# Optimization experiments

Hardware: AMD Instinct MI355X
Metric: run time of the kernel (lower is better)

The kernel has to match this reference:

```python
import jax, jax.numpy as jnp
import numpy as np

NUM_CLASSES = 2
LOG2_NC = float(np.log2(NUM_CLASSES))


def _conv(x, w, b=None):
    # NCHW conv, stride 1, SAME padding (kernel 3 pad 1 or kernel 1 pad 0)
    y = jax.lax.conv_general_dilated(x, w, (1, 1), 'SAME',
                                     dimension_numbers=('NCHW', 'OIHW', 'NCHW'))
    if b is not None:
        y = y + b[None, :, None, None]
    return y


def _uncertainty_map(ds):
    # entropy over class dim, thresholded to {0,1}
    logp = jax.nn.log_softmax(ds, axis=1)            # [B,C,H,W]
    prob = jnp.exp(logp)
    # torch uses log2(prob + 1e-6); replicate exactly
    ent = -jnp.sum(prob * jnp.log2(prob + 1e-6), axis=1) / LOG2_NC  # [B,H,W]
    return (ent >= 0.001).astype(jnp.float32)


def _unob(tar, amap):
    # vectorized UnoB with S=3: interior pixels with tar!=0 get pro=0 unless
    # 4*tar == sum of the 4-neighborhood (i.e. locally constant label)
    t = tar  # [B,H,W] int
    nb = t[:, 2:, 1:-1] + t[:, :-2, 1:-1] + t[:, 1:-1, 2:] + t[:, 1:-1, :-2]
    center = t[:, 1:-1, 1:-1]
    inner_pro = jnp.where((center != 0) & (4 * center != nb), 0.0, 1.0)
    pro = jnp.ones_like(amap)
    pro = pro.at[:, 1:-1, 1:-1].set(inner_pro)
    return amap * pro


def setup_inputs() -> dict:
    key = jax.random.key(0)
    ks = jax.random.split(key, 6)
    B, C, H, W = 8, 128, 128, 128
    return {
        'x': jax.random.normal(ks[0], (B, C, H, W), jnp.float32),
        'skip': jax.random.normal(ks[1], (B, C, H, W), jnp.float32),
        'tar': jax.random.randint(ks[2], (B, 1, H, W), 0, NUM_CLASSES, jnp.int64)
            if jax.config.jax_enable_x64 else
            jax.random.randint(ks[2], (B, 1, H, W), 0, NUM_CLASSES).astype(jnp.int32),
        'W1': jax.random.normal(ks[3], (128, 256, 3, 3), jnp.float32) * 0.05,
        'b1': jnp.zeros((128,), jnp.float32),
        'W2': jax.random.normal(ks[4], (128, 128, 3, 3), jnp.float32) * 0.05,
        'b2': jnp.zeros((128,), jnp.float32),
        'Wds': jax.random.normal(ks[5], (NUM_CLASSES, 128, 1, 1), jnp.float32) * 0.05,
    }


def reference(x, skip, tar, W1, b1, W2, b2, Wds):
    h = jnp.concatenate([x, skip], axis=1)            # [B,2*dim,H,W]
    h = jax.nn.leaky_relu(_conv(h, W1, b1), 0.01)     # [B,dim,H,W]
    h = jax.nn.leaky_relu(_conv(h, W2, b2), 0.01)
    ds = _conv(h, Wds)                                # [B,num_classes,H,W]
    amap = _uncertainty_map(ds)                       # [B,H,W]
    amap = _unob(tar[:, 0], amap)                     # UnoB refinement, S=3
    return h, ds, amap
```

## Files before the change

### kernel.cpp

```cpp
#include <hip/hip_runtime.h>

typedef float f32x16 __attribute__((ext_vector_type(16)));
typedef short bf16x8 __attribute__((ext_vector_type(8)));
typedef unsigned int u32;

static __device__ __forceinline__ unsigned short f2bf(float f) {
  union { float f; unsigned int u; } v;
  v.f = f;
  return (unsigned short)((v.u + 0x7FFFu + ((v.u >> 16) & 1u)) >> 16);
}

static __device__ __forceinline__ void gl_lds16(const unsigned short* g,
                                                unsigned short* l) {
  __builtin_amdgcn_global_load_lds(
      (const __attribute__((address_space(1))) u32*)g,
      (__attribute__((address_space(3))) u32*)l, 16, 0, 0);
}

#define VMCNT8 asm volatile("s_waitcnt vmcnt(8)" ::: "memory")
#define VMCNT0 asm volatile("s_waitcnt vmcnt(0)" ::: "memory")
#define LGKM0 asm volatile("s_waitcnt lgkmcnt(0)" ::: "memory")
#define BAR __builtin_amdgcn_s_barrier()
#define SCHEDB __builtin_amdgcn_sched_barrier(0)
#define PRIO1 __builtin_amdgcn_s_setprio(1)
#define PRIO0 __builtin_amdgcn_s_setprio(0)

__global__ __launch_bounds__(256) void convert_weights(
    const float* __restrict__ W1, const float* __restrict__ W2,
    unsigned short* __restrict__ W1b, unsigned short* __restrict__ W2b,
    unsigned short* __restrict__ zp) {
  if (blockIdx.x == 1728) {
    uint4* z = (uint4*)zp;
    z[threadIdx.x] = make_uint4(0, 0, 0, 0);
    z[256 + threadIdx.x] = make_uint4(0, 0, 0, 0);
    return;
  }
  int i = blockIdx.x * 256 + threadIdx.x;
  if (i < 294912) {
    int e = i & 7, co = (i >> 3) & 127, r = i >> 10;
    int tap = r % 9, pc = r / 9;
    int ci = (pc >> 1) * 16 + (pc & 1) * 8 + e;
    W1b[i] = f2bf(W1[(co * 256 + ci) * 9 + tap]);
  } else {
    int j = i - 294912;
    if (j < 147456) {
      int e = j & 7, co = (j >> 3) & 127, r = j >> 10;
      int tap = r % 9, pc = r / 9;
      int ci = (pc >> 1) * 16 + (pc & 1) * 8 + e;
      W2b[j] = f2bf(W2[(co * 128 + ci) * 9 + tap]);
    }
  }
}

__global__ __launch_bounds__(256) void transpose_to_bf16(
    const float* __restrict__ src, unsigned short* __restrict__ dst, int cigb) {
  int row = blockIdx.x;
  int b = row >> 7, y = row & 127;
  const float* s = src + (long)b * 128 * 16384 + (long)y * 128;
  for (int it = 0; it < 8; ++it) {
    int u = it * 256 + (int)threadIdx.x;
    int cig = u >> 7, px = u & 127;
    unsigned short pk[8];
#pragma unroll
    for (int e = 0; e < 8; ++e)
      pk[e] = f2bf(s[(long)(cig * 8 + e) * 16384 + px]);
    uint4 vv;
    vv.x = (unsigned)pk[0] | ((unsigned)pk[1] << 16);
    vv.y = (unsigned)pk[2] | ((unsigned)pk[3] << 16);
    vv.z = (unsigned)pk[4] | ((unsigned)pk[5] << 16);
    vv.w = (unsigned)pk[6] | ((unsigned)pk[7] << 16);
    *(uint4*)(&dst[(((long)row * 32 + cigb + cig) * 130 + px + 1) * 8]) = vv;
  }
  if (cigb == 0 && threadIdx.x < 64) {
    int g = threadIdx.x >> 1;
    long col = (threadIdx.x & 1) * 129L;
    *(uint4*)(&dst[(((long)row * 32 + g) * 130 + col) * 8]) = make_uint4(0, 0, 0, 0);
  }
}

template <int CIN, bool FUSE_DS>
__global__ __launch_bounds__(512, 2) void conv3x3(
    const unsigned short* __restrict__ src,
    const unsigned short* __restrict__ wt,
    const float* __restrict__ bias,
    const unsigned short* __restrict__ zp,
    unsigned short* __restrict__ dst_bf16,
    float* __restrict__ dst_f32,
    const float* __restrict__ wds,
    const int* __restrict__ tar,
    float* __restrict__ ds,
    float* __restrict__ amap) {
  constexpr int CPG = CIN / 8;
  constexpr int NC = CIN / 16;
  __shared__ unsigned short in_tile[2][1664 * 8];
  __shared__ unsigned short wt_tile[2][2304 * 8];
  __shared__ unsigned short scr[64 * 8];
  __shared__ float sb[128];
  __shared__ float w0s[128], w1s[128];
  __shared__ float sc[4 * 4 * 2 * 32];

  const int tid = threadIdx.x;
  const int b = blockIdx.x >> 5;
  const int y0 = (blockIdx.x & 31) * 4;
  const int lane = tid & 63, wave = tid >> 6;
  const int wco = wave & 1, wrow = wave >> 1;
  const int l31 = lane & 31, kh = lane >> 5;

  if (tid < 128) {
    sb[tid] = bias[tid];
    if constexpr (FUSE_DS) {
      w0s[tid] = wds[tid];
      w1s[tid] = wds[128 + tid];
    }
  }

  const unsigned short* gb[8];
  unsigned short* ld0[8];
  int gst[8];
  int lst[8];
#pragma unroll
  for (int i = 0; i < 8; ++i) {
    const int o = wave * 8 + i;
    if (o < 36) {
      gb[i] = wt + o * 512 + lane * 8;
      gst[i] = 18432;
      ld0[i] = &wt_tile[0][(size_t)o * 512];
      lst[i] = 18432;
    } else if (o < 62) {
      const int q = o - 36;
      const int p = q / 13, j = q - p * 13;
      const int s = j * 64 + lane;
      const int hy = s / 130, hx = s - hy * 130;
      const int gy = y0 - 1 + hy;
      const bool ok = (s < 780) && (gy >= 0) && (gy < 128);
      gb[i] = ok ? src + ((size_t)((b * 128 + gy) * CPG) + p) * 1040 + hx * 8
                 : zp + lane * 8;
      gst[i] = ok ? 2080 : 0;
      ld0[i] = &in_tile[0][(size_t)(p * 832 + j * 64) * 8];
      lst[i] = 1664 * 8;
    } else {
      gb[i] = zp + lane * 8;
      gst[i] = 0;
      ld0[i] = &scr[0];
      lst[i] = 0;
    }
  }

  f32x16 acc[2][4] = {};

#pragma unroll
  for (int i = 0; i < 8; ++i) gl_lds16(gb[i], ld0[i]);
  VMCNT0;
  LGKM0;
  BAR;
  SCHEDB;

  for (int cic = 0; cic < NC; ++cic) {
    const int cur = cic & 1;
    const bool more = (cic + 1 < NC);
    if (more) {
      const int nb = cur ^ 1;
#pragma unroll
      for (int i = 0; i < 8; ++i)
        gl_lds16(gb[i] + (size_t)(cic + 1) * gst[i],
                 ld0[i] + (size_t)nb * lst[i]);
      SCHEDB;
      VMCNT8;
    } else {
      VMCNT0;
    }
    SCHEDB;
    BAR;
    SCHEDB;

    const unsigned short* it = &in_tile[cur][0];
    const unsigned short* wl = &wt_tile[cur][0];
    const size_t ib = (size_t)kh * (832 * 8);
    const size_t wb = (size_t)kh * 9216;

    bf16x8 xa0, xa1, xb0, xb1, xb2, xb3;
    bf16x8 ya0, ya1, yb0, yb1, yb2, yb3;

#define LD_TAP(T, A0, A1, B0, B1, B2, B3)                                      \
  {                                                                            \
    constexpr int ky_ = (T) / 3, kx_ = (T) % 3;                                \
    const int hy_ = ky_ + wrow;                                                \
    A0 = *(const bf16x8*)(&wl[wb + (size_t)((T)*128 + wco * 64 + l31) * 8]);   \
    A1 = *(const bf16x8*)(&wl[wb + (size_t)((T)*128 + wco * 64 + 32 + l31) * 8]); \
    B0 = *(const bf16x8*)(&it[ib + (size_t)(hy_ * 130 + l31 + kx_) * 8]);      \
    B1 = *(const bf16x8*)(&it[ib + (size_t)(hy_ * 130 + 32 + l31 + kx_) * 8]); \
    B2 = *(const bf16x8*)(&it[ib + (size_t)(hy_ * 130 + 64 + l31 + kx_) * 8]); \
    B3 = *(const bf16x8*)(&it[ib + (size_t)(hy_ * 130 + 96 + l31 + kx_) * 8]); \
  }

#define MFMA_TAP(A0, A1, B0, B1, B2, B3)                                       \
  {                                                                            \
    PRIO1;                                                                     \
    acc[0][0] = __builtin_amdgcn_mfma_f32_32x32x16_bf16(A0, B0, acc[0][0], 0, 0, 0); \
    acc[0][1] = __builtin_amdgcn_mfma_f32_32x32x16_bf16(A0, B1, acc[0][1], 0, 0, 0); \
    acc[0][2] = __builtin_amdgcn_mfma_f32_32x32x16_bf16(A0, B2, acc[0][2], 0, 0, 0); \
    acc[0][3] = __builtin_amdgcn_mfma_f32_32x32x16_bf16(A0, B3, acc[0][3], 0, 0, 0); \
    acc[1][0] = __builtin_amdgcn_mfma_f32_32x32x16_bf16(A1, B0, acc[1][0], 0, 0, 0); \
    acc[1][1] = __builtin_amdgcn_mfma_f32_32x32x16_bf16(A1, B1, acc[1][1], 0, 0, 0); \
    acc[1][2] = __builtin_amdgcn_mfma_f32_32x32x16_bf16(A1, B2, acc[1][2], 0, 0, 0); \
    acc[1][3] = __builtin_amdgcn_mfma_f32_32x32x16_bf16(A1, B3, acc[1][3], 0, 0, 0); \
    PRIO0;                                                                     \
  }

    LD_TAP(0, xa0, xa1, xb0, xb1, xb2, xb3);
    LD_TAP(1, ya0, ya1, yb0, yb1, yb2, yb3);
    SCHEDB;
    MFMA_TAP(xa0, xa1, xb0, xb1, xb2, xb3);
    LD_TAP(2, xa0, xa1, xb0, xb1, xb2, xb3);
    SCHEDB;
    MFMA_TAP(ya0, ya1, yb0, yb1, yb2, yb3);
    LD_TAP(3, ya0, ya1, yb0, yb1, yb2, yb3);
    SCHEDB;
    MFMA_TAP(xa0, xa1, xb0, xb1, xb2, xb3);
    LD_TAP(4, xa0, xa1, xb0, xb1, xb2, xb3);
    SCHEDB;
    MFMA_TAP(ya0, ya1, yb0, yb1, yb2, yb3);
    LD_TAP(5, ya0, ya1, yb0, yb1, yb2, yb3);
    SCHEDB;
    MFMA_TAP(xa0, xa1, xb0, xb1, xb2, xb3);
    LD_TAP(6, xa0, xa1, xb0, xb1, xb2, xb3);
    SCHEDB;
    MFMA_TAP(ya0, ya1, yb0, yb1, yb2, yb3);
    LD_TAP(7, ya0, ya1, yb0, yb1, yb2, yb3);
    SCHEDB;
    MFMA_TAP(xa0, xa1, xb0, xb1, xb2, xb3);
    LD_TAP(8, xa0, xa1, xb0, xb1, xb2, xb3);
    SCHEDB;
    MFMA_TAP(ya0, ya1, yb0, yb1, yb2, yb3);
    SCHEDB;
    MFMA_TAP(xa0, xa1, xb0, xb1, xb2, xb3);
#undef LD_TAP
#undef MFMA_TAP

    SCHEDB;
    LGKM0;
    BAR;
    SCHEDB;
  }

  const int gyo = y0 + wrow;
  float pd[4][2] = {};
#pragma unroll
  for (int fc = 0; fc < 2; ++fc) {
#pragma unroll
    for (int fp = 0; fp < 4; ++fp) {
      const int px = fp * 32 + l31;
      if constexpr (!FUSE_DS) {
#pragma unroll
        for (int rg = 0; rg < 4; ++rg) {
          const int co0 = wco * 64 + fc * 32 + rg * 8 + kh * 4;
          unsigned short pk[4];
#pragma unroll
          for (int q = 0; q < 4; ++q) {
            float v = acc[fc][fp][rg * 4 + q] + sb[co0 + q];
            v = v > 0.f ? v : 0.01f * v;
            pk[q] = f2bf(v);
          }
          uint2 o;
          o.x = (unsigned)pk[0] | ((unsigned)pk[1] << 16);
          o.y = (unsigned)pk[2] | ((unsigned)pk[3] << 16);
          *(uint2*)(&dst_bf16[(((long)(b * 128 + gyo) * 16 + (co0 >> 3)) * 130 + px + 1) * 8 +
                              kh * 4]) = o;
        }
      } else {
#pragma unroll
        for (int rg = 0; rg < 4; ++rg) {
          const int co0 = wco * 64 + fc * 32 + rg * 8 + kh * 4;
          float4 wv0 = *(const float4*)(&w0s[co0]);
          float4 wv1 = *(const float4*)(&w1s[co0]);
#pragma unroll
          for (int q = 0; q < 4; ++q) {
            float v = acc[fc][fp][rg * 4 + q] + sb[co0 + q];
            v = v > 0.f ? v : 0.01f * v;
            dst_f32[((long)(b * 128 + co0 + q) << 14) + (gyo << 7) + px] = v;
            float wq0 = (q == 0) ? wv0.x : (q == 1) ? wv0.y : (q == 2) ? wv0.z : wv0.w;
            float wq1 = (q == 0) ? wv1.x : (q == 1) ? wv1.y : (q == 2) ? wv1.z : wv1.w;
            pd[fp][0] += wq0 * v;
            pd[fp][1] += wq1 * v;
          }
        }
      }
    }
  }

  if constexpr (!FUSE_DS) {
    if (tid < 128) {
      int row = tid >> 5, g = (tid >> 1) & 15;
      long col = (tid & 1) * 129L;
      *(uint4*)(&dst_bf16[(((long)(b * 128 + y0 + row) * 16 + g) * 130 + col) * 8]) =
          make_uint4(0, 0, 0, 0);
    }
  } else {
#pragma unroll
    for (int fp = 0; fp < 4; ++fp)
#pragma unroll
      for (int c = 0; c < 2; ++c)
        pd[fp][c] += __shfl_xor(pd[fp][c], 32, 64);
    if (wco == 1 && kh == 0) {
#pragma unroll
      for (int fp = 0; fp < 4; ++fp)
#pragma unroll
        for (int c = 0; c < 2; ++c)
          sc[((wrow * 4 + fp) * 2 + c) * 32 + l31] = pd[fp][c];
    }
    __syncthreads();
    if (wco == 0 && kh == 0) {
      const int* tb = tar + (long)b * 16384;
#pragma unroll
      for (int fp = 0; fp < 4; ++fp) {
        const int px = fp * 32 + l31;
        float a0 = pd[fp][0] + sc[((wrow * 4 + fp) * 2 + 0) * 32 + l31];
        float a1 = pd[fp][1] + sc[((wrow * 4 + fp) * 2 + 1) * 32 + l31];
        ds[((long)b * 2) * 16384 + (gyo << 7) + px] = a0;
        ds[((long)b * 2 + 1) * 16384 + (gyo << 7) + px] = a1;
        float m = fmaxf(a0, a1);
        float e0 = expf(a0 - m), e1 = expf(a1 - m);
        float s = e0 + e1;
        float p0f = e0 / s, p1f = e1 / s;
        float ent = -(p0f * log2f(p0f + 1e-6f) + p1f * log2f(p1f + 1e-6f));
        float un = ent >= 0.001f ? 1.f : 0.f;
        float pro = 1.f;
        if (gyo > 0 && gyo < 127 && px > 0 && px < 127) {
          int c = tb[(gyo << 7) + px];
          if (c != 0) {
            int nb2 = tb[((gyo - 1) << 7) + px] + tb[((gyo + 1) << 7) + px] +
                      tb[(gyo << 7) + px - 1] + tb[(gyo << 7) + px + 1];
            if (4 * c != nb2) pro = 0.f;
          }
        }
        amap[((long)(b * 128 + gyo) << 7) + px] = un * pro;
      }
    }
  }
}

extern "C" void kernel_launch(void* const* d_in, const int* in_sizes, int n_in,
                              void* d_out, int out_size, void* d_ws, size_t ws_size,
                              hipStream_t stream) {
  const float* x    = (const float*)d_in[0];
  const float* skip = (const float*)d_in[1];
  const int*   tar  = (const int*)d_in[2];
  const float* W1   = (const float*)d_in[3];
  const float* b1   = (const float*)d_in[4];
  const float* W2   = (const float*)d_in[5];
  const float* b2   = (const float*)d_in[6];
  const float* Wds  = (const float*)d_in[7];

  float* out_h  = (float*)d_out;
  float* out_ds = out_h + 16777216;
  float* out_am = out_ds + 262144;

  unsigned short* W1b = (unsigned short*)d_ws;
  unsigned short* W2b = W1b + 294912;
  unsigned short* zp  = W2b + 147456;
  unsigned short* h1  = (unsigned short*)((char*)d_ws + (1u << 20));

  unsigned short* h0 = (unsigned short*)d_out;

  convert_weights<<<1729, 256, 0, stream>>>(W1, W2, W1b, W2b, zp);
  transpose_to_bf16<<<1024, 256, 0, stream>>>(x, h0, 0);
  transpose_to_bf16<<<1024, 256, 0, stream>>>(skip, h0, 16);
  conv3x3<256, false><<<256, 512, 0, stream>>>(h0, W1b, b1, zp, h1, nullptr,
                                               nullptr, nullptr, nullptr, nullptr);
  conv3x3<128, true><<<256, 512, 0, stream>>>(h1, W2b, b2, zp, nullptr, out_h,
                                              Wds, tar, out_ds, out_am);
}
```

Before: 149.3 us.

## Restructure conv prefetch pipeline, merge transpose launches, remap workgroups across XCDs

The next chunk's global-to-LDS prefetch now goes out in two halves interleaved with the MFMA taps. Barriers sit between tap groups and the wait for outstanding loads moves to the end of the iteration, so load latency hides behind compute. The two transpose launches are merged into one grid, and conv workgroup IDs are permuted so that adjacent rows of the same batch land on the same XCD. The extra barriers and the changed priority placement add synchronisation cost per iteration.

```diff
diff --git a/kernel.cpp b/kernel.cpp
--- a/kernel.cpp
+++ b/kernel.cpp
@@ -17,7 +17,6 @@
       (__attribute__((address_space(3))) u32*)l, 16, 0, 0);
 }
 
-#define VMCNT8 asm volatile("s_waitcnt vmcnt(8)" ::: "memory")
 #define VMCNT0 asm volatile("s_waitcnt vmcnt(0)" ::: "memory")
 #define LGKM0 asm volatile("s_waitcnt lgkmcnt(0)" ::: "memory")
 #define BAR __builtin_amdgcn_s_barrier()
@@ -53,8 +52,12 @@
 }
 
 __global__ __launch_bounds__(256) void transpose_to_bf16(
-    const float* __restrict__ src, unsigned short* __restrict__ dst, int cigb) {
-  int row = blockIdx.x;
+    const float* __restrict__ x, const float* __restrict__ skip,
+    unsigned short* __restrict__ dst) {
+  int bid = blockIdx.x;
+  const float* src = (bid < 1024) ? x : skip;
+  int cigb = (bid < 1024) ? 0 : 16;
+  int row = bid & 1023;
   int b = row >> 7, y = row & 127;
   const float* s = src + (long)b * 128 * 16384 + (long)y * 128;
   for (int it = 0; it < 8; ++it) {
@@ -100,8 +103,9 @@
   __shared__ float sc[4 * 4 * 2 * 32];
 
   const int tid = threadIdx.x;
-  const int b = blockIdx.x >> 5;
-  const int y0 = (blockIdx.x & 31) * 4;
+  const int wg = (blockIdx.x & 7) * 32 + (blockIdx.x >> 3);
+  const int b = wg >> 5;
+  const int y0 = (wg & 31) * 4;
   const int lane = tid & 63, wave = tid >> 6;
   const int wco = wave & 1, wrow = wave >> 1;
   const int l31 = lane & 31, kh = lane >> 5;
@@ -157,21 +161,8 @@
 
   for (int cic = 0; cic < NC; ++cic) {
     const int cur = cic & 1;
+    const int nbuf = cur ^ 1;
     const bool more = (cic + 1 < NC);
-    if (more) {
-      const int nb = cur ^ 1;
-#pragma unroll
-      for (int i = 0; i < 8; ++i)
-        gl_lds16(gb[i] + (size_t)(cic + 1) * gst[i],
-                 ld0[i] + (size_t)nb * lst[i]);
-      SCHEDB;
-      VMCNT8;
-    } else {
-      VMCNT0;
-    }
-    SCHEDB;
-    BAR;
-    SCHEDB;
 
     const unsigned short* it = &in_tile[cur][0];
     const unsigned short* wl = &wt_tile[cur][0];
@@ -195,7 +186,6 @@
 
 #define MFMA_TAP(A0, A1, B0, B1, B2, B3)                                       \
   {                                                                            \
-    PRIO1;                                                                     \
     acc[0][0] = __builtin_amdgcn_mfma_f32_32x32x16_bf16(A0, B0, acc[0][0], 0, 0, 0); \
     acc[0][1] = __builtin_amdgcn_mfma_f32_32x32x16_bf16(A0, B1, acc[0][1], 0, 0, 0); \
     acc[0][2] = __builtin_amdgcn_mfma_f32_32x32x16_bf16(A0, B2, acc[0][2], 0, 0, 0); \
@@ -204,12 +194,21 @@
     acc[1][1] = __builtin_amdgcn_mfma_f32_32x32x16_bf16(A1, B1, acc[1][1], 0, 0, 0); \
     acc[1][2] = __builtin_amdgcn_mfma_f32_32x32x16_bf16(A1, B2, acc[1][2], 0, 0, 0); \
     acc[1][3] = __builtin_amdgcn_mfma_f32_32x32x16_bf16(A1, B3, acc[1][3], 0, 0, 0); \
-    PRIO0;                                                                     \
   }
 
     LD_TAP(0, xa0, xa1, xb0, xb1, xb2, xb3);
     LD_TAP(1, ya0, ya1, yb0, yb1, yb2, yb3);
     SCHEDB;
+
+    if (more) {
+#pragma unroll
+      for (int i = 0; i < 4; ++i)
+        gl_lds16(gb[i] + (size_t)(cic + 1) * gst[i],
+                 ld0[i] + (size_t)nbuf * lst[i]);
+    }
+    SCHEDB;
+    BAR;
+    PRIO1;
     MFMA_TAP(xa0, xa1, xb0, xb1, xb2, xb3);
     LD_TAP(2, xa0, xa1, xb0, xb1, xb2, xb3);
     SCHEDB;
@@ -219,6 +218,17 @@
     MFMA_TAP(xa0, xa1, xb0, xb1, xb2, xb3);
     LD_TAP(4, xa0, xa1, xb0, xb1, xb2, xb3);
     SCHEDB;
+    PRIO0;
+
+    if (more) {
+#pragma unroll
+      for (int i = 4; i < 8; ++i)
+        gl_lds16(gb[i] + (size_t)(cic + 1) * gst[i],
+                 ld0[i] + (size_t)nbuf * lst[i]);
+    }
+    SCHEDB;
+    BAR;
+    PRIO1;
     MFMA_TAP(ya0, ya1, yb0, yb1, yb2, yb3);
     LD_TAP(5, ya0, ya1, yb0, yb1, yb2, yb3);
     SCHEDB;
@@ -228,17 +238,23 @@
     MFMA_TAP(ya0, ya1, yb0, yb1, yb2, yb3);
     LD_TAP(7, ya0, ya1, yb0, yb1, yb2, yb3);
     SCHEDB;
+    PRIO0;
+
+    BAR;
+    PRIO1;
     MFMA_TAP(xa0, xa1, xb0, xb1, xb2, xb3);
     LD_TAP(8, xa0, xa1, xb0, xb1, xb2, xb3);
     SCHEDB;
     MFMA_TAP(ya0, ya1, yb0, yb1, yb2, yb3);
     SCHEDB;
     MFMA_TAP(xa0, xa1, xb0, xb1, xb2, xb3);
+    PRIO0;
 #undef LD_TAP
 #undef MFMA_TAP
 
     SCHEDB;
     LGKM0;
+    VMCNT0;
     BAR;
     SCHEDB;
   }
@@ -363,8 +379,7 @@
   unsigned short* h0 = (unsigned short*)d_out;
 
   convert_weights<<<1729, 256, 0, stream>>>(W1, W2, W1b, W2b, zp);
-  transpose_to_bf16<<<1024, 256, 0, stream>>>(x, h0, 0);
-  transpose_to_bf16<<<1024, 256, 0, stream>>>(skip, h0, 16);
+  transpose_to_bf16<<<2048, 256, 0, stream>>>(x, skip, h0);
   conv3x3<256, false><<<256, 512, 0, stream>>>(h0, W1b, b1, zp, h1, nullptr,
                                                nullptr, nullptr, nullptr, nullptr);
   conv3x3<128, true><<<256, 512, 0, stream>>>(h1, W2b, b2, zp, nullptr, out_h,
```

Result: no change. 147.3 us (-1.4%).
